# Kernel optimization log

Hardware: AMD Instinct MI355X
Metric: run time of the kernel (lower is better)

Reference implementation:

```python
import jax, jax.numpy as jnp
import numpy as np

HID = 2048          # hidden_size
INTER = 4096        # expand * hidden_size
NH = 64             # num_heads
HD = 64             # head_dim (NH*HD == INTER)
N = 128             # ssm state_size
G = 1               # n_groups
K = 4               # conv_kernel
EPS = 1e-5
CONV_DIM = INTER + 2 * G * N            # 4352
PROJ = INTER + CONV_DIM + NH            # 8512 (d_mlp == 0)


def setup_inputs() -> dict:
    key = jax.random.key(0)
    ks = jax.random.split(key, 6)
    B, S = 2, 2048
    return {
        "hidden_states": jax.random.normal(ks[0], (B, S, HID), jnp.float32),
        "in_proj_w": jax.random.normal(ks[1], (PROJ, HID), jnp.float32) * 0.02,
        "conv_w": jax.random.normal(ks[2], (CONV_DIM, 1, K), jnp.float32) * 0.1,
        "conv_b": jax.random.normal(ks[3], (CONV_DIM,), jnp.float32) * 0.02,
        "dt_bias": jnp.ones((NH,), jnp.float32),
        "A_log": jnp.log(jnp.arange(1, NH + 1, dtype=jnp.float32)),
        "D": jnp.ones((NH,), jnp.float32),
        "norm_weight": jnp.ones((INTER,), jnp.float32),
        "out_proj_w": jax.random.normal(ks[4], (HID, INTER), jnp.float32) * 0.02,
    }


def _mamba2_forward(hidden_states, in_proj_w, conv_w, conv_b, dt_bias,
                    A_log, D, norm_weight, out_proj_w):
    b, sq, _ = hidden_states.shape
    # in_proj (d_mlp == 0, so split is gate | hidden_B_C | dt)
    proj = hidden_states @ in_proj_w.T                       # [b, s, PROJ]
    gate, hbc, dt = jnp.split(proj, [INTER, INTER + CONV_DIM], axis=-1)

    # causal depthwise conv1d over time + SiLU
    xc = jnp.transpose(hbc, (0, 2, 1))                       # [b, conv_dim, s]
    xc = jax.lax.conv_general_dilated(xc, conv_w, (1,), [(K - 1, 0)],
                                      feature_group_count=CONV_DIM)
    xc = xc + conv_b[None, :, None]
    hbc = jax.nn.silu(jnp.transpose(xc, (0, 2, 1)))          # [b, s, conv_dim]

    hs, Bm, Cm = jnp.split(hbc, [INTER, INTER + G * N], axis=-1)
    hs = hs.reshape(b, sq, NH, HD)
    Bm = jnp.repeat(Bm.reshape(b, sq, G, N), NH // G, axis=2)   # [b, s, nh, n]
    Cm = jnp.repeat(Cm.reshape(b, sq, G, N), NH // G, axis=2)

    A = -jnp.exp(A_log)                                      # [nh]
    dt = jax.nn.softplus(dt + dt_bias)                       # [b, s, nh]

    # selective SSM scan: state_t = exp(dt*A)*state_{t-1} + dt*B_t x_t^T
    def step(state, inp):
        xt, Bt, Ct, dtt = inp                                # [b,nh,hd],[b,nh,n],[b,nh,n],[b,nh]
        dA = jnp.exp(dtt * A)                                # [b, nh]
        state = state * dA[..., None, None] \
            + (dtt[..., None] * xt)[..., None] * Bt[:, :, None, :]
        y = jnp.einsum('bhdn,bhn->bhd', state, Ct)
        return state, y

    init = jnp.zeros((b, NH, HD, N), jnp.float32)
    xs = (jnp.moveaxis(hs, 1, 0), jnp.moveaxis(Bm, 1, 0),
          jnp.moveaxis(Cm, 1, 0), jnp.moveaxis(dt, 1, 0))
    _, ys = jax.lax.scan(step, init, xs)                     # [s, b, nh, hd]
    y = jnp.moveaxis(ys, 0, 1) + D[None, None, :, None] * hs
    y = y.reshape(b, sq, INTER)

    # gated RMSNorm (norm_before_gate=False): gate first, then normalize
    y = y * jax.nn.silu(gate)
    var = jnp.mean(y * y, axis=-1, keepdims=True)
    y = y * jax.lax.rsqrt(var + EPS) * norm_weight
    return y @ out_proj_w.T                                  # [b, s, HID]


def reference(hidden_states, in_proj_w, conv_w, conv_b, dt_bias, A_log, D,
              norm_weight, out_proj_w):
    return _mamba2_forward(hidden_states, in_proj_w, conv_w, conv_b, dt_bias,
                           A_log, D, norm_weight, out_proj_w)
```

## Files before the change

kernel.cpp:

```cpp
#include <hip/hip_runtime.h>
#include <hip/hip_bf16.h>
#include <cstddef>
#include <cstdint>

#define HID   2048
#define INTER 4096
#define NH    64
#define HD    64
#define NST   128
#define CONV_DIM 4352
#define PROJ  8512
#define PROJ_PAD 8704
#define SS    2048
#define BB    2
#define BS    (BB*SS)
#define EPS   1e-5f

#define COL_HS 4096
#define COL_B  8192
#define COL_C  8320
#define COL_DT 8448

#define NCHC  64
#define CHUNKC 32
#define CV8   (CONV_DIM / 8)

#define CL    128
#define NCHK  16

typedef short s16x8 __attribute__((ext_vector_type(8)));
typedef float f32x4 __attribute__((ext_vector_type(4)));

__device__ inline ushort f2b(float x) {
  __hip_bfloat16 h = __float2bfloat16(x);
  return *(ushort*)&h;
}
__device__ inline float b2f(ushort u) {
  unsigned int v = ((unsigned int)u) << 16;
  return __uint_as_float(v);
}
__device__ inline int swz(int row, int e) { return row * 128 + (e ^ ((row & 7) << 3)); }

__device__ inline void gload16(const void* g, void* l) {
  __builtin_amdgcn_global_load_lds((const __attribute__((address_space(1))) void*)g,
                                   (__attribute__((address_space(3))) void*)l, 16, 0, 0);
}

#define N4A  ((long)BS * HID / 4)
#define N4W1 ((long)PROJ_PAD * HID / 4)
#define N4W2 ((long)HID * INTER / 4)

__global__ __launch_bounds__(256) void convert_all(
    const float* __restrict__ hs, const float* __restrict__ w1,
    const float* __restrict__ w2, ushort* __restrict__ hs16,
    ushort* __restrict__ w1p, ushort* __restrict__ w216) {
  long i = (long)blockIdx.x * 256 + threadIdx.x;
  const float* src;
  ushort* dst;
  long e0;
  if (i < N4A) {
    src = hs; dst = hs16; e0 = i * 4;
  } else if (i < N4A + N4W1) {
    long k = i - N4A;
    e0 = k * 4;
    long row = e0 >> 11;
    if (row >= PROJ) {
      ushort4 z = {0, 0, 0, 0};
      *(ushort4*)(w1p + e0) = z;
      return;
    }
    src = w1; dst = w1p;
  } else if (i < N4A + N4W1 + N4W2) {
    long k = i - N4A - N4W1;
    src = w2; dst = w216; e0 = k * 4;
  } else {
    return;
  }
  float4 v = *(const float4*)(src + e0);
  ushort4 o;
  o.x = f2b(v.x); o.y = f2b(v.y); o.z = f2b(v.z); o.w = f2b(v.w);
  *(ushort4*)(dst + e0) = o;
}

__global__ __launch_bounds__(512, 2) void gemm1_256x128(
    const ushort* __restrict__ A, const ushort* __restrict__ Bw,
    ushort* __restrict__ C, float* __restrict__ dtbuf) {
  __shared__ ushort smem[49152];
  const int tid = threadIdx.x;
  const int lane = tid & 63;
  const int wid = tid >> 6;
  const int wm = wid >> 1;
  const int wn = wid & 1;
  const int r = lane & 15;
  const int kx = lane >> 4;

  const int fid = blockIdx.x;
  const int rg = fid / 272;
  const int ix = fid % 272;
  const int brow = rg * 4 + (ix & 3);
  const int bcol = ix >> 2;

  const ushort* Ag = A + (size_t)(brow * 256) * HID;
  const ushort* Bg = Bw + (size_t)(bcol * 128) * HID;

  const int srow = tid >> 3;
  const int scole = (((tid & 7) * 16) ^ ((srow & 7) << 4)) >> 1;

  auto stageA1 = [&](int buf, int kt) {
#pragma unroll
    for (int i = 0; i < 4; i++) {
      gload16(Ag + (size_t)(i * 64 + srow) * HID + kt * 64 + scole,
              smem + buf * 16384 + i * 4096 + tid * 8);
    }
  };
  auto stageB1 = [&](int buf, int kt) {
#pragma unroll
    for (int i = 0; i < 2; i++) {
      gload16(Bg + (size_t)(i * 64 + srow) * HID + kt * 64 + scole,
              smem + 32768 + buf * 8192 + i * 4096 + tid * 8);
    }
  };
  auto ldA1 = [&](int buf, int mf, int ks) -> s16x8 {
    int row = wm * 64 + mf * 16 + r;
    int cb = (ks * 64 + kx * 16) ^ ((row & 7) << 4);
    return *(const s16x8*)(smem + buf * 16384 + row * 64 + (cb >> 1));
  };
  auto ldB1 = [&](int buf, int nf, int ks) -> s16x8 {
    int row = wn * 64 + nf * 16 + r;
    int cb = (ks * 64 + kx * 16) ^ ((row & 7) << 4);
    return *(const s16x8*)(smem + 32768 + buf * 8192 + row * 64 + (cb >> 1));
  };

  f32x4 acc[4][4];
#pragma unroll
  for (int i = 0; i < 4; i++)
#pragma unroll
    for (int j = 0; j < 4; j++) acc[i][j] = (f32x4)0.f;

  constexpr int NT = HID / 64;

  stageA1(0, 0); stageB1(0, 0);
  stageA1(1, 1); stageB1(1, 1);
  asm volatile("s_waitcnt vmcnt(6)" ::: "memory");
  __builtin_amdgcn_s_barrier();

  int cur = 0;
  for (int t = 0; t < NT; t++) {
    s16x8 a[4][2], b[4][2];
#pragma unroll
    for (int mf = 0; mf < 4; mf++)
#pragma unroll
      for (int ks = 0; ks < 2; ks++) a[mf][ks] = ldA1(cur, mf, ks);
#pragma unroll
    for (int nf = 0; nf < 4; nf++)
#pragma unroll
      for (int ks = 0; ks < 2; ks++) b[nf][ks] = ldB1(cur, nf, ks);
    __builtin_amdgcn_s_barrier();
    asm volatile("s_waitcnt lgkmcnt(0)" ::: "memory");
    __builtin_amdgcn_sched_barrier(0);
    __builtin_amdgcn_s_setprio(1);
#pragma unroll
    for (int mf = 0; mf < 4; mf++)
#pragma unroll
      for (int nf = 0; nf < 2; nf++)
#pragma unroll
        for (int ks = 0; ks < 2; ks++)
          acc[mf][nf] = __builtin_amdgcn_mfma_f32_16x16x32_bf16(a[mf][ks], b[nf][ks], acc[mf][nf], 0, 0, 0);
    __builtin_amdgcn_s_setprio(0);
    __builtin_amdgcn_s_barrier();
    if (t + 2 < NT) { stageA1(cur, t + 2); stageB1(cur, t + 2); }
    __builtin_amdgcn_s_setprio(1);
#pragma unroll
    for (int mf = 0; mf < 4; mf++)
#pragma unroll
      for (int nf = 2; nf < 4; nf++)
#pragma unroll
        for (int ks = 0; ks < 2; ks++)
          acc[mf][nf] = __builtin_amdgcn_mfma_f32_16x16x32_bf16(a[mf][ks], b[nf][ks], acc[mf][nf], 0, 0, 0);
    __builtin_amdgcn_s_setprio(0);
    if (t + 2 < NT) {
      asm volatile("s_waitcnt vmcnt(6)" ::: "memory");
    } else {
      asm volatile("s_waitcnt vmcnt(0)" ::: "memory");
    }
    __builtin_amdgcn_s_barrier();
    cur ^= 1;
  }

  const int m0 = brow * 256 + wm * 64 + (lane >> 4) * 4;
  const int n0 = bcol * 128 + wn * 64 + r;
#pragma unroll
  for (int mf = 0; mf < 4; mf++) {
#pragma unroll
    for (int nf = 0; nf < 4; nf++) {
      int n = n0 + nf * 16;
      if (n >= PROJ) continue;
#pragma unroll
      for (int q = 0; q < 4; q++) {
        float v = acc[mf][nf][q];
        int m = m0 + mf * 16 + q;
        C[(size_t)m * PROJ + n] = f2b(v);
        if (n >= COL_DT) dtbuf[(size_t)m * 64 + (n - COL_DT)] = v;
      }
    }
  }
}

__global__ __launch_bounds__(512, 2) void gemm2_256x128(
    const ushort* __restrict__ A, const ushort* __restrict__ Bw,
    float* __restrict__ C) {
  __shared__ ushort smem[49152];
  const int tid = threadIdx.x;
  const int lane = tid & 63;
  const int wid = tid >> 6;
  const int wm = wid >> 1;
  const int wn = wid & 1;
  const int r = lane & 15;
  const int kx = lane >> 4;

  const int fid = blockIdx.x;
  const int bcol = fid >> 4;
  const int brow = fid & 15;

  const ushort* Ag = A + (size_t)(brow * 256) * PROJ;
  const ushort* Bg = Bw + (size_t)(bcol * 128) * INTER;

  const int srow = tid >> 3;
  const int scole = (((tid & 7) * 16) ^ ((srow & 7) << 4)) >> 1;

  auto stageA2 = [&](int buf, int kt) {
#pragma unroll
    for (int i = 0; i < 4; i++) {
      gload16(Ag + (size_t)(i * 64 + srow) * PROJ + kt * 64 + scole,
              smem + buf * 16384 + i * 4096 + tid * 8);
    }
  };
  auto stageB2 = [&](int buf, int kt) {
#pragma unroll
    for (int i = 0; i < 2; i++) {
      gload16(Bg + (size_t)(i * 64 + srow) * INTER + kt * 64 + scole,
              smem + 32768 + buf * 8192 + i * 4096 + tid * 8);
    }
  };
  auto ldA2 = [&](int buf, int mf, int ks) -> s16x8 {
    int row = wm * 64 + mf * 16 + r;
    int cb = (ks * 64 + kx * 16) ^ ((row & 7) << 4);
    return *(const s16x8*)(smem + buf * 16384 + row * 64 + (cb >> 1));
  };
  auto ldB2 = [&](int buf, int nf, int ks) -> s16x8 {
    int row = wn * 64 + nf * 16 + r;
    int cb = (ks * 64 + kx * 16) ^ ((row & 7) << 4);
    return *(const s16x8*)(smem + 32768 + buf * 8192 + row * 64 + (cb >> 1));
  };

  f32x4 acc[4][4];
#pragma unroll
  for (int i = 0; i < 4; i++)
#pragma unroll
    for (int j = 0; j < 4; j++) acc[i][j] = (f32x4)0.f;

  constexpr int NT = INTER / 64;

  stageA2(0, 0); stageB2(0, 0);
  stageA2(1, 1); stageB2(1, 1);
  asm volatile("s_waitcnt vmcnt(6)" ::: "memory");
  __builtin_amdgcn_s_barrier();

  int cur = 0;
  for (int t = 0; t < NT; t++) {
    s16x8 a[4][2], b[4][2];
#pragma unroll
    for (int mf = 0; mf < 4; mf++)
#pragma unroll
      for (int ks = 0; ks < 2; ks++) a[mf][ks] = ldA2(cur, mf, ks);
#pragma unroll
    for (int nf = 0; nf < 4; nf++)
#pragma unroll
      for (int ks = 0; ks < 2; ks++) b[nf][ks] = ldB2(cur, nf, ks);
    __builtin_amdgcn_s_barrier();
    asm volatile("s_waitcnt lgkmcnt(0)" ::: "memory");
    __builtin_amdgcn_sched_barrier(0);
    __builtin_amdgcn_s_setprio(1);
#pragma unroll
    for (int mf = 0; mf < 4; mf++)
#pragma unroll
      for (int nf = 0; nf < 2; nf++)
#pragma unroll
        for (int ks = 0; ks < 2; ks++)
          acc[mf][nf] = __builtin_amdgcn_mfma_f32_16x16x32_bf16(a[mf][ks], b[nf][ks], acc[mf][nf], 0, 0, 0);
    __builtin_amdgcn_s_setprio(0);
    __builtin_amdgcn_s_barrier();
    if (t + 2 < NT) { stageA2(cur, t + 2); stageB2(cur, t + 2); }
    __builtin_amdgcn_s_setprio(1);
#pragma unroll
    for (int mf = 0; mf < 4; mf++)
#pragma unroll
      for (int nf = 2; nf < 4; nf++)
#pragma unroll
        for (int ks = 0; ks < 2; ks++)
          acc[mf][nf] = __builtin_amdgcn_mfma_f32_16x16x32_bf16(a[mf][ks], b[nf][ks], acc[mf][nf], 0, 0, 0);
    __builtin_amdgcn_s_setprio(0);
    if (t + 2 < NT) {
      asm volatile("s_waitcnt vmcnt(6)" ::: "memory");
    } else {
      asm volatile("s_waitcnt vmcnt(0)" ::: "memory");
    }
    __builtin_amdgcn_s_barrier();
    cur ^= 1;
  }

  const int m0 = brow * 256 + wm * 64 + (lane >> 4) * 4;
  const int n0 = bcol * 128 + wn * 64 + r;
#pragma unroll
  for (int mf = 0; mf < 4; mf++) {
#pragma unroll
    for (int nf = 0; nf < 4; nf++) {
      int n = n0 + nf * 16;
#pragma unroll
      for (int q = 0; q < 4; q++)
        C[(size_t)(m0 + mf * 16 + q) * HID + n] = acc[mf][nf][q];
    }
  }
}

__global__ __launch_bounds__(256) void conv_capture(
    const ushort* __restrict__ proj, ushort* __restrict__ side) {
  int idx = blockIdx.x * 256 + threadIdx.x;
  const int total = BB * NCHC * 3 * CV8;
  if (idx >= total) return;
  int c8 = idx % CV8;
  int t = idx / CV8;
  int j = t % 3; t /= 3;
  int chunk = t % NCHC;
  int b = t / NCHC;
  int s = chunk * CHUNKC - 1 - j;
  s16x8 v = {0, 0, 0, 0, 0, 0, 0, 0};
  if (s >= 0) v = *(const s16x8*)(proj + ((size_t)b * SS + s) * PROJ + COL_HS + c8 * 8);
  *(s16x8*)(side + ((size_t)(b * NCHC + chunk) * 3 + j) * CONV_DIM + c8 * 8) = v;
}

__global__ __launch_bounds__(256) void conv_silu(
    ushort* __restrict__ proj, const ushort* __restrict__ side,
    const float* __restrict__ cw, const float* __restrict__ cb) {
  int idx = blockIdx.x * 256 + threadIdx.x;
  const int total = BB * NCHC * CV8;
  if (idx >= total) return;
  int c8 = idx % CV8;
  int t = idx / CV8;
  int chunk = t % NCHC;
  int b = t / NCHC;
  const int c0 = c8 * 8;
  float w0[8], w1[8], w2[8], w3[8], bias[8], h1[8], h2[8], h3[8];
#pragma unroll
  for (int e = 0; e < 8; e++) {
    float4 wv = *(const float4*)(cw + (c0 + e) * 4);
    w0[e] = wv.x; w1[e] = wv.y; w2[e] = wv.z; w3[e] = wv.w;
    bias[e] = cb[c0 + e];
  }
  const ushort* sd = side + (size_t)(b * NCHC + chunk) * 3 * CONV_DIM;
  {
    s16x8 v1 = *(const s16x8*)(sd + c0);
    s16x8 v2 = *(const s16x8*)(sd + CONV_DIM + c0);
    s16x8 v3 = *(const s16x8*)(sd + 2 * CONV_DIM + c0);
#pragma unroll
    for (int e = 0; e < 8; e++) {
      h1[e] = b2f((ushort)v1[e]);
      h2[e] = b2f((ushort)v2[e]);
      h3[e] = b2f((ushort)v3[e]);
    }
  }
  size_t p = ((size_t)b * SS + (size_t)chunk * CHUNKC) * PROJ + COL_HS + c0;
  for (int s = 0; s < CHUNKC; s++) {
    s16x8 xv = *(const s16x8*)(proj + p);
    s16x8 ov;
#pragma unroll
    for (int e = 0; e < 8; e++) {
      float x = b2f((ushort)xv[e]);
      float o = w3[e] * x + w2[e] * h1[e] + w1[e] * h2[e] + w0[e] * h3[e] + bias[e];
      o = o / (1.f + __expf(-o));
      ov[e] = (short)f2b(o);
      h3[e] = h2[e]; h2[e] = h1[e]; h1[e] = x;
    }
    *(s16x8*)(proj + p) = ov;
    p += PROJ;
  }
}

__global__ __launch_bounds__(256) void ssd_chunk_state(
    const ushort* __restrict__ proj, const float* __restrict__ dtf,
    const float* __restrict__ dt_bias, const float* __restrict__ A_log,
    ushort* __restrict__ states, float* __restrict__ cumbuf,
    float* __restrict__ dtvbuf) {
  const int bid = blockIdx.x;
  const int c = bid & 15;
  const int h = (bid >> 4) & 63;
  const int b = bid >> 10;
  const int tid = threadIdx.x;
  const int lane = tid & 63;
  const int wv = tid >> 6;
  __shared__ float sdtv[CL], scum[CL], sw[CL];
  __shared__ ushort sBt[128 * 128];
  __shared__ ushort sXw[64 * 128];
  const size_t row0 = (size_t)b * SS + (size_t)c * CL;
  const size_t bh = (size_t)(b * NH + h);

  const float Ah = -__expf(A_log[h]);
  if (tid < CL) {
    float z = dtf[(row0 + tid) * 64 + h] + dt_bias[h];
    float dtv = (z > 20.f) ? z : log1pf(__expf(z));
    sdtv[tid] = dtv;
    sw[tid] = dtv * Ah;
  }
  __syncthreads();
  for (int off = 1; off < CL; off <<= 1) {
    float v = 0.f;
    if (tid < CL) { v = sw[tid]; if (tid >= off) v += sw[tid - off]; }
    __syncthreads();
    if (tid < CL) sw[tid] = v;
    __syncthreads();
  }
  if (tid < CL) {
    scum[tid] = sw[tid];
    cumbuf[bh * SS + c * CL + tid] = sw[tid];
    dtvbuf[bh * SS + c * CL + tid] = sdtv[tid];
  }
  __syncthreads();
  const float cumL = scum[CL - 1];
  if (tid < CL) sw[tid] = __expf(cumL - scum[tid]) * sdtv[tid];
  __syncthreads();

  {
    const int t = tid >> 1, n0 = (tid & 1) * 64;
    const ushort* src = proj + (row0 + t) * PROJ + COL_B + n0;
#pragma unroll
    for (int j = 0; j < 64; j += 8) {
      s16x8 v = *(const s16x8*)(src + j);
#pragma unroll
      for (int e = 0; e < 8; e++) sBt[swz(n0 + j + e, t)] = (ushort)v[e];
    }
  }
  {
    const int d = tid & 63;
    const int t0 = (tid >> 6) * 32;
    for (int t = t0; t < t0 + 32; t++) {
      float x = b2f(proj[(row0 + t) * PROJ + COL_HS + h * 64 + d]);
      sXw[swz(d, t)] = f2b(x * sw[t]);
    }
  }
  __syncthreads();

  const int r = lane & 15, kx = lane >> 4;
  f32x4 acc[2][4];
#pragma unroll
  for (int i = 0; i < 2; i++)
#pragma unroll
    for (int j = 0; j < 4; j++) acc[i][j] = (f32x4)0.f;
#pragma unroll
  for (int kk = 0; kk < 4; kk++) {
    s16x8 a[2], bo[4];
#pragma unroll
    for (int i = 0; i < 2; i++)
      a[i] = *(const s16x8*)&sBt[swz(wv * 32 + i * 16 + r, kk * 32 + kx * 8)];
#pragma unroll
    for (int j = 0; j < 4; j++)
      bo[j] = *(const s16x8*)&sXw[swz(j * 16 + r, kk * 32 + kx * 8)];
#pragma unroll
    for (int i = 0; i < 2; i++)
#pragma unroll
      for (int j = 0; j < 4; j++)
        acc[i][j] = __builtin_amdgcn_mfma_f32_16x16x32_bf16(a[i], bo[j], acc[i][j], 0, 0, 0);
  }
  ushort* dst = states + (size_t)bid * (128 * 64);
#pragma unroll
  for (int i = 0; i < 2; i++) {
#pragma unroll
    for (int j = 0; j < 4; j++) {
      int n = wv * 32 + i * 16 + (lane >> 4) * 4;
      int d = (lane & 15) + j * 16;
      ushort4 o;
      o.x = f2b(acc[i][j][0]);
      o.y = f2b(acc[i][j][1]);
      o.z = f2b(acc[i][j][2]);
      o.w = f2b(acc[i][j][3]);
      *(ushort4*)(dst + (size_t)d * 128 + n) = o;
    }
  }
}

__global__ __launch_bounds__(256) void ssd_state_scan(
    ushort* __restrict__ states, const float* __restrict__ cumbuf) {
  const int bh = blockIdx.x;
  const int tid = threadIdx.x;
  float run[32];
#pragma unroll
  for (int i = 0; i < 32; i++) run[i] = 0.f;
  for (int c = 0; c < NCHK; c++) {
    float dec = __expf(cumbuf[(size_t)bh * SS + c * CL + (CL - 1)]);
    ushort* p = states + ((size_t)bh * NCHK + c) * 8192 + tid * 32;
    s16x8 in[4];
#pragma unroll
    for (int v = 0; v < 4; v++) in[v] = *(const s16x8*)(p + v * 8);
    s16x8 out[4];
#pragma unroll
    for (int v = 0; v < 4; v++) {
#pragma unroll
      for (int e = 0; e < 8; e++) {
        int i = v * 8 + e;
        out[v][e] = (short)f2b(run[i]);
        run[i] = dec * run[i] + b2f((ushort)in[v][e]);
      }
    }
#pragma unroll
    for (int v = 0; v < 4; v++) *(s16x8*)(p + v * 8) = out[v];
  }
}

__global__ __launch_bounds__(256, 2) void ssd_chunk_out(
    ushort* __restrict__ proj, const ushort* __restrict__ states,
    const float* __restrict__ cumbuf, const float* __restrict__ dtvbuf,
    const float* __restrict__ Dp) {
  const int bid = blockIdx.x;
  const int c = bid & 15;
  const int h = (bid >> 4) & 63;
  const int b = bid >> 10;
  const int tid = threadIdx.x;
  const int lane = tid & 63;
  const int wv = tid >> 6;
  __shared__ ushort sC[128 * 128];
  __shared__ ushort sB[128 * 128];
  __shared__ ushort sX[64 * 128];
  const size_t row0 = (size_t)b * SS + (size_t)c * CL;
  const size_t bh = (size_t)(b * NH + h);
  const float* cumb = cumbuf + bh * SS + c * CL;
  const float* dtvb = dtvbuf + bh * SS + c * CL;
  const int r = lane & 15, kx = lane >> 4;

  float ct[2][4];
#pragma unroll
  for (int i = 0; i < 2; i++)
#pragma unroll
    for (int q = 0; q < 4; q++)
      ct[i][q] = cumb[wv * 32 + i * 16 + ((lane >> 4) << 2) + q];
  float cumt[8], dvt[8];
#pragma unroll
  for (int j = 0; j < 8; j++) {
    int tau = j * 16 + (lane & 15);
    cumt[j] = cumb[tau];
    dvt[j] = dtvb[tau];
  }
  const float eC = __expf(cumb[wv * 32 + (lane >> 1)]);

  {
    const int t = tid >> 1, n0 = (tid & 1) * 64;
    const ushort* srcC = proj + (row0 + t) * PROJ + COL_C + n0;
    const ushort* srcB = proj + (row0 + t) * PROJ + COL_B + n0;
#pragma unroll
    for (int j = 0; j < 64; j += 8) {
      *(s16x8*)&sC[swz(t, n0 + j)] = *(const s16x8*)(srcC + j);
      *(s16x8*)&sB[swz(t, n0 + j)] = *(const s16x8*)(srcB + j);
    }
  }
  {
    const int d = tid & 63;
    const int t0 = (tid >> 6) * 32;
    for (int t = t0; t < t0 + 32; t++)
      sX[swz(d, t)] = proj[(row0 + t) * PROJ + COL_HS + h * 64 + d];
  }
  __syncthreads();

  f32x4 g[2][8];
#pragma unroll
  for (int i = 0; i < 2; i++)
#pragma unroll
    for (int j = 0; j < 8; j++) g[i][j] = (f32x4)0.f;
#pragma unroll
  for (int kk = 0; kk < 4; kk++) {
    s16x8 a[2], bo[8];
#pragma unroll
    for (int i = 0; i < 2; i++)
      a[i] = *(const s16x8*)&sC[swz(wv * 32 + i * 16 + r, kk * 32 + kx * 8)];
#pragma unroll
    for (int j = 0; j < 8; j++)
      bo[j] = *(const s16x8*)&sB[swz(j * 16 + r, kk * 32 + kx * 8)];
#pragma unroll
    for (int i = 0; i < 2; i++)
#pragma unroll
      for (int j = 0; j < 8; j++)
        g[i][j] = __builtin_amdgcn_mfma_f32_16x16x32_bf16(a[i], bo[j], g[i][j], 0, 0, 0);
  }

  s16x8 spf[4][4];
  {
    const ushort* sp = states + (size_t)bid * 8192;
#pragma unroll
    for (int kk = 0; kk < 4; kk++)
#pragma unroll
      for (int j = 0; j < 4; j++)
        spf[kk][j] = *(const s16x8*)(sp + (size_t)(j * 16 + r) * 128 + kk * 32 + kx * 8);
  }
  __syncthreads();

#pragma unroll
  for (int j = 0; j < 8; j++) {
    float cu = cumt[j], dv = dvt[j];
    int tau = j * 16 + (lane & 15);
#pragma unroll
    for (int i = 0; i < 2; i++) {
#pragma unroll
      for (int q = 0; q < 4; q++) {
        int t = wv * 32 + i * 16 + ((lane >> 4) << 2) + q;
        float val = (tau <= t) ? g[i][j][q] * __expf(ct[i][q] - cu) * dv : 0.f;
        sB[swz(t, tau)] = f2b(val);
      }
    }
  }
  {
    int t = wv * 32 + (lane >> 1);
    int n0 = (lane & 1) * 64;
#pragma unroll
    for (int j = 0; j < 64; j += 8) {
      s16x8 u = *(const s16x8*)&sC[swz(t, n0 + j)];
#pragma unroll
      for (int k = 0; k < 8; k++) u[k] = (short)f2b(b2f((ushort)u[k]) * eC);
      *(s16x8*)&sC[swz(t, n0 + j)] = u;
    }
  }
  __syncthreads();

  f32x4 y[2][4];
#pragma unroll
  for (int i = 0; i < 2; i++)
#pragma unroll
    for (int j = 0; j < 4; j++) y[i][j] = (f32x4)0.f;
#pragma unroll
  for (int kk = 0; kk < 4; kk++) {
    s16x8 a[2], bo[4];
#pragma unroll
    for (int i = 0; i < 2; i++)
      a[i] = *(const s16x8*)&sB[swz(wv * 32 + i * 16 + r, kk * 32 + kx * 8)];
#pragma unroll
    for (int j = 0; j < 4; j++)
      bo[j] = *(const s16x8*)&sX[swz(j * 16 + r, kk * 32 + kx * 8)];
#pragma unroll
    for (int i = 0; i < 2; i++)
#pragma unroll
      for (int j = 0; j < 4; j++)
        y[i][j] = __builtin_amdgcn_mfma_f32_16x16x32_bf16(a[i], bo[j], y[i][j], 0, 0, 0);
  }
#pragma unroll
  for (int kk = 0; kk < 4; kk++) {
    s16x8 a[2];
#pragma unroll
    for (int i = 0; i < 2; i++)
      a[i] = *(const s16x8*)&sC[swz(wv * 32 + i * 16 + r, kk * 32 + kx * 8)];
#pragma unroll
    for (int i = 0; i < 2; i++)
#pragma unroll
      for (int j = 0; j < 4; j++)
        y[i][j] = __builtin_amdgcn_mfma_f32_16x16x32_bf16(a[i], spf[kk][j], y[i][j], 0, 0, 0);
  }

  const float Dh = Dp[h];
#pragma unroll
  for (int i = 0; i < 2; i++) {
#pragma unroll
    for (int j = 0; j < 4; j++) {
      int t0 = wv * 32 + i * 16 + (lane >> 4) * 4;
      int d = (lane & 15) + j * 16;
#pragma unroll
      for (int q = 0; q < 4; q++) {
        float x = b2f(sX[swz(d, t0 + q)]);
        proj[(row0 + t0 + q) * PROJ + COL_HS + h * 64 + d] = f2b(y[i][j][q] + Dh * x);
      }
    }
  }
}

__global__ __launch_bounds__(256) void rmsnorm_kernel(
    ushort* __restrict__ proj, const float* __restrict__ nw) {
  const int row = blockIdx.x;
  const int tid = threadIdx.x;
  ushort* yp = proj + (size_t)row * PROJ + COL_HS;
  const ushort* gp = proj + (size_t)row * PROJ;
  float v[16];
  float ss = 0.f;
#pragma unroll
  for (int q = 0; q < 4; q++) {
    int col = q * 1024 + tid * 4;
    ushort4 yv = *(const ushort4*)(yp + col);
    ushort4 gv = *(const ushort4*)(gp + col);
    float vy[4] = {b2f(yv.x), b2f(yv.y), b2f(yv.z), b2f(yv.w)};
    float vg[4] = {b2f(gv.x), b2f(gv.y), b2f(gv.z), b2f(gv.w)};
#pragma unroll
    for (int j = 0; j < 4; j++) {
      float sg = vg[j] / (1.f + __expf(-vg[j]));
      float vv = vy[j] * sg;
      v[q * 4 + j] = vv;
      ss += vv * vv;
    }
  }
#pragma unroll
  for (int o = 1; o < 64; o <<= 1) ss += __shfl_xor(ss, o);
  __shared__ float red[4];
  if ((tid & 63) == 0) red[tid >> 6] = ss;
  __syncthreads();
  float tot = red[0] + red[1] + red[2] + red[3];
  float scale = rsqrtf(tot * (1.f / INTER) + EPS);
#pragma unroll
  for (int q = 0; q < 4; q++) {
    int col = q * 1024 + tid * 4;
    float4 w = *(const float4*)(nw + col);
    ushort4 o;
    o.x = f2b(v[q * 4 + 0] * scale * w.x);
    o.y = f2b(v[q * 4 + 1] * scale * w.y);
    o.z = f2b(v[q * 4 + 2] * scale * w.z);
    o.w = f2b(v[q * 4 + 3] * scale * w.w);
    *(ushort4*)(yp + col) = o;
  }
}

extern "C" void kernel_launch(void* const* d_in, const int* in_sizes, int n_in,
                              void* d_out, int out_size, void* d_ws, size_t ws_size,
                              hipStream_t stream) {
  const float* hs   = (const float*)d_in[0];
  const float* w1   = (const float*)d_in[1];
  const float* cw   = (const float*)d_in[2];
  const float* cb   = (const float*)d_in[3];
  const float* dtb  = (const float*)d_in[4];
  const float* alog = (const float*)d_in[5];
  const float* Dp   = (const float*)d_in[6];
  const float* nw   = (const float*)d_in[7];
  const float* w2   = (const float*)d_in[8];
  float* out = (float*)d_out;

  char* base = (char*)d_ws;
  size_t off = 0;
  ushort* proj = (ushort*)(base + off); off += (size_t)BS * PROJ * 2;
  ushort* side = (ushort*)(base + off); off += (size_t)BB * NCHC * 3 * CONV_DIM * 2;
  off = (off + 255) & ~(size_t)255;
  float* dtbuf = (float*)(base + off); off += (size_t)BS * 64 * 4;
  off = (off + 255) & ~(size_t)255;
  ushort* w216 = (ushort*)(base + off); off += (size_t)HID * INTER * 2;
  off = (off + 255) & ~(size_t)255;
  char* rC = base + off;
  ushort* hs16 = (ushort*)rC;
  ushort* w1p  = (ushort*)(rC + 16777216);
  ushort* states = (ushort*)rC;
  float*  cumbuf = (float*)(rC + 33554432);
  float*  dtvbuf = (float*)(rC + 33554432 + 1048576);

  {
    long n4 = N4A + N4W1 + N4W2;
    convert_all<<<(int)((n4 + 255) / 256), 256, 0, stream>>>(hs, w1, w2, hs16, w1p, w216);
  }

  gemm1_256x128<<<1088, 512, 0, stream>>>(hs16, w1p, proj, dtbuf);

  conv_capture<<<(BB * NCHC * 3 * CV8 + 255) / 256, 256, 0, stream>>>(proj, side);
  conv_silu<<<(BB * NCHC * CV8 + 255) / 256, 256, 0, stream>>>(proj, side, cw, cb);

  ssd_chunk_state<<<BB * NH * NCHK, 256, 0, stream>>>(proj, dtbuf, dtb, alog, states, cumbuf, dtvbuf);
  ssd_state_scan<<<BB * NH, 256, 0, stream>>>(states, cumbuf);
  ssd_chunk_out<<<BB * NH * NCHK, 256, 0, stream>>>(proj, states, cumbuf, dtvbuf, Dp);

  rmsnorm_kernel<<<BS, 256, 0, stream>>>(proj, nw);

  gemm2_256x128<<<256, 512, 0, stream>>>(
      (const ushort*)(proj + COL_HS), w216, out);
}
```

Measured before the change: 440.1 us.

## Enlarge in_proj GEMM tile to 256x256, wave-shuffle dt scan, register C in chunk_out

The in_proj GEMM moves from 256x128 to 256x256 tiles with 8 waves in a 2x4 layout and an 8-phase schedule that interleaves LDS reads, MFMA groups and staged global loads. This raises arithmetic intensity per block and halves the grid. The chunk-state kernel swaps its barrier-heavy shared-memory prefix sum for wave shuffles. The chunk-output kernel loads C fragments directly into registers, drops the sC shared buffer and the rescale pass, and applies exp(cum) to a separate inter-chunk accumulator in fp32. The larger tile uses more LDS and accumulator registers, which may reduce occupancy.

```diff
diff --git a/kernel.cpp b/kernel.cpp
--- a/kernel.cpp
+++ b/kernel.cpp
@@ -82,79 +82,77 @@
   *(ushort4*)(dst + e0) = o;
 }
 
-__global__ __launch_bounds__(512, 2) void gemm1_256x128(
+__global__ __launch_bounds__(512, 2) void gemm256_8ph(
     const ushort* __restrict__ A, const ushort* __restrict__ Bw,
     ushort* __restrict__ C, float* __restrict__ dtbuf) {
-  __shared__ ushort smem[49152];
+  __shared__ ushort smem[65536];
   const int tid = threadIdx.x;
   const int lane = tid & 63;
   const int wid = tid >> 6;
-  const int wm = wid >> 1;
-  const int wn = wid & 1;
+  const int wm = wid >> 2;
+  const int wn = wid & 3;
   const int r = lane & 15;
   const int kx = lane >> 4;
 
   const int fid = blockIdx.x;
-  const int rg = fid / 272;
-  const int ix = fid % 272;
-  const int brow = rg * 4 + (ix & 3);
-  const int bcol = ix >> 2;
+  const int bcol = ((fid >> 7) << 3) + ((fid & 127) >> 4);
+  const int brow = fid & 15;
 
   const ushort* Ag = A + (size_t)(brow * 256) * HID;
-  const ushort* Bg = Bw + (size_t)(bcol * 128) * HID;
+  const ushort* Bg = Bw + (size_t)(bcol * 256) * HID;
 
   const int srow = tid >> 3;
   const int scole = (((tid & 7) * 16) ^ ((srow & 7) << 4)) >> 1;
 
-  auto stageA1 = [&](int buf, int kt) {
-#pragma unroll
-    for (int i = 0; i < 4; i++) {
-      gload16(Ag + (size_t)(i * 64 + srow) * HID + kt * 64 + scole,
-              smem + buf * 16384 + i * 4096 + tid * 8);
-    }
+  auto stageA = [&](int buf, int kt, int half) {
+    const ushort* g = Ag + (size_t)(half * 128 + srow) * HID + kt * 64 + scole;
+    ushort* l = smem + buf * 16384 + half * 8192 + tid * 8;
+    gload16(g, l);
+    gload16(g + (size_t)64 * HID, l + 4096);
   };
-  auto stageB1 = [&](int buf, int kt) {
-#pragma unroll
-    for (int i = 0; i < 2; i++) {
-      gload16(Bg + (size_t)(i * 64 + srow) * HID + kt * 64 + scole,
-              smem + 32768 + buf * 8192 + i * 4096 + tid * 8);
-    }
+  auto stageB = [&](int buf, int kt, int half) {
+    const ushort* g = Bg + (size_t)(half * 128 + srow) * HID + kt * 64 + scole;
+    ushort* l = smem + 32768 + buf * 16384 + half * 8192 + tid * 8;
+    gload16(g, l);
+    gload16(g + (size_t)64 * HID, l + 4096);
   };
-  auto ldA1 = [&](int buf, int mf, int ks) -> s16x8 {
-    int row = wm * 64 + mf * 16 + r;
+  auto ldA = [&](int buf, int mf, int ks) -> s16x8 {
+    int row = wm * 128 + mf * 16 + r;
     int cb = (ks * 64 + kx * 16) ^ ((row & 7) << 4);
     return *(const s16x8*)(smem + buf * 16384 + row * 64 + (cb >> 1));
   };
-  auto ldB1 = [&](int buf, int nf, int ks) -> s16x8 {
+  auto ldB = [&](int buf, int nf, int ks) -> s16x8 {
     int row = wn * 64 + nf * 16 + r;
     int cb = (ks * 64 + kx * 16) ^ ((row & 7) << 4);
-    return *(const s16x8*)(smem + 32768 + buf * 8192 + row * 64 + (cb >> 1));
+    return *(const s16x8*)(smem + 32768 + buf * 16384 + row * 64 + (cb >> 1));
   };
 
-  f32x4 acc[4][4];
-#pragma unroll
-  for (int i = 0; i < 4; i++)
+  f32x4 acc[8][4];
+#pragma unroll
+  for (int i = 0; i < 8; i++)
 #pragma unroll
     for (int j = 0; j < 4; j++) acc[i][j] = (f32x4)0.f;
 
   constexpr int NT = HID / 64;
 
-  stageA1(0, 0); stageB1(0, 0);
-  stageA1(1, 1); stageB1(1, 1);
-  asm volatile("s_waitcnt vmcnt(6)" ::: "memory");
+  stageA(0, 0, 0); stageA(0, 0, 1);
+  stageB(0, 0, 0); stageB(0, 0, 1);
+  stageA(1, 1, 0); stageA(1, 1, 1);
+  asm volatile("s_waitcnt vmcnt(4)" ::: "memory");
   __builtin_amdgcn_s_barrier();
 
   int cur = 0;
   for (int t = 0; t < NT; t++) {
-    s16x8 a[4][2], b[4][2];
-#pragma unroll
-    for (int mf = 0; mf < 4; mf++)
-#pragma unroll
-      for (int ks = 0; ks < 2; ks++) a[mf][ks] = ldA1(cur, mf, ks);
-#pragma unroll
-    for (int nf = 0; nf < 4; nf++)
-#pragma unroll
-      for (int ks = 0; ks < 2; ks++) b[nf][ks] = ldB1(cur, nf, ks);
+    s16x8 a[4][2], b[2][2], b2[2][2];
+#pragma unroll
+    for (int mf = 0; mf < 4; mf++)
+#pragma unroll
+      for (int ks = 0; ks < 2; ks++) a[mf][ks] = ldA(cur, mf, ks);
+#pragma unroll
+    for (int nf = 0; nf < 2; nf++)
+#pragma unroll
+      for (int ks = 0; ks < 2; ks++) b[nf][ks] = ldB(cur, nf, ks);
+    if (t + 1 < NT) stageB(cur ^ 1, t + 1, 0);
     __builtin_amdgcn_s_barrier();
     asm volatile("s_waitcnt lgkmcnt(0)" ::: "memory");
     __builtin_amdgcn_sched_barrier(0);
@@ -168,18 +166,53 @@
           acc[mf][nf] = __builtin_amdgcn_mfma_f32_16x16x32_bf16(a[mf][ks], b[nf][ks], acc[mf][nf], 0, 0, 0);
     __builtin_amdgcn_s_setprio(0);
     __builtin_amdgcn_s_barrier();
-    if (t + 2 < NT) { stageA1(cur, t + 2); stageB1(cur, t + 2); }
+#pragma unroll
+    for (int nf = 0; nf < 2; nf++)
+#pragma unroll
+      for (int ks = 0; ks < 2; ks++) b2[nf][ks] = ldB(cur, nf + 2, ks);
+    if (t + 1 < NT) stageB(cur ^ 1, t + 1, 1);
+    __builtin_amdgcn_s_barrier();
+    asm volatile("s_waitcnt lgkmcnt(0)" ::: "memory");
+    __builtin_amdgcn_sched_barrier(0);
     __builtin_amdgcn_s_setprio(1);
 #pragma unroll
     for (int mf = 0; mf < 4; mf++)
 #pragma unroll
-      for (int nf = 2; nf < 4; nf++)
+      for (int nf = 0; nf < 2; nf++)
 #pragma unroll
         for (int ks = 0; ks < 2; ks++)
-          acc[mf][nf] = __builtin_amdgcn_mfma_f32_16x16x32_bf16(a[mf][ks], b[nf][ks], acc[mf][nf], 0, 0, 0);
+          acc[mf][nf + 2] = __builtin_amdgcn_mfma_f32_16x16x32_bf16(a[mf][ks], b2[nf][ks], acc[mf][nf + 2], 0, 0, 0);
+    __builtin_amdgcn_s_setprio(0);
+    __builtin_amdgcn_s_barrier();
+#pragma unroll
+    for (int mf = 0; mf < 4; mf++)
+#pragma unroll
+      for (int ks = 0; ks < 2; ks++) a[mf][ks] = ldA(cur, mf + 4, ks);
+    __builtin_amdgcn_s_barrier();
+    asm volatile("s_waitcnt lgkmcnt(0)" ::: "memory");
+    __builtin_amdgcn_sched_barrier(0);
+    __builtin_amdgcn_s_setprio(1);
+#pragma unroll
+    for (int mf = 0; mf < 4; mf++)
+#pragma unroll
+      for (int nf = 0; nf < 2; nf++)
+#pragma unroll
+        for (int ks = 0; ks < 2; ks++)
+          acc[mf + 4][nf] = __builtin_amdgcn_mfma_f32_16x16x32_bf16(a[mf][ks], b[nf][ks], acc[mf + 4][nf], 0, 0, 0);
+    __builtin_amdgcn_s_setprio(0);
+    __builtin_amdgcn_s_barrier();
+    if (t + 2 < NT) { stageA(cur, t + 2, 0); stageA(cur, t + 2, 1); }
+    __builtin_amdgcn_s_setprio(1);
+#pragma unroll
+    for (int mf = 0; mf < 4; mf++)
+#pragma unroll
+      for (int nf = 0; nf < 2; nf++)
+#pragma unroll
+        for (int ks = 0; ks < 2; ks++)
+          acc[mf + 4][nf + 2] = __builtin_amdgcn_mfma_f32_16x16x32_bf16(a[mf][ks], b2[nf][ks], acc[mf + 4][nf + 2], 0, 0, 0);
     __builtin_amdgcn_s_setprio(0);
     if (t + 2 < NT) {
-      asm volatile("s_waitcnt vmcnt(6)" ::: "memory");
+      asm volatile("s_waitcnt vmcnt(4)" ::: "memory");
     } else {
       asm volatile("s_waitcnt vmcnt(0)" ::: "memory");
     }
@@ -187,10 +220,10 @@
     cur ^= 1;
   }
 
-  const int m0 = brow * 256 + wm * 64 + (lane >> 4) * 4;
-  const int n0 = bcol * 128 + wn * 64 + r;
-#pragma unroll
-  for (int mf = 0; mf < 4; mf++) {
+  const int m0 = brow * 256 + wm * 128 + (lane >> 4) * 4;
+  const int n0 = bcol * 256 + wn * 64 + r;
+#pragma unroll
+  for (int mf = 0; mf < 8; mf++) {
 #pragma unroll
     for (int nf = 0; nf < 4; nf++) {
       int n = n0 + nf * 16;
@@ -399,34 +432,36 @@
   const int lane = tid & 63;
   const int wv = tid >> 6;
   __shared__ float sdtv[CL], scum[CL], sw[CL];
+  __shared__ float wtot[2];
   __shared__ ushort sBt[128 * 128];
   __shared__ ushort sXw[64 * 128];
   const size_t row0 = (size_t)b * SS + (size_t)c * CL;
   const size_t bh = (size_t)(b * NH + h);
 
   const float Ah = -__expf(A_log[h]);
+  float dtvv = 0.f, v = 0.f;
   if (tid < CL) {
     float z = dtf[(row0 + tid) * 64 + h] + dt_bias[h];
-    float dtv = (z > 20.f) ? z : log1pf(__expf(z));
-    sdtv[tid] = dtv;
-    sw[tid] = dtv * Ah;
-  }
+    dtvv = (z > 20.f) ? z : log1pf(__expf(z));
+    v = dtvv * Ah;
+  }
+#pragma unroll
+  for (int off = 1; off < 64; off <<= 1) {
+    float u = __shfl_up(v, off);
+    if (lane >= off) v += u;
+  }
+  if (tid < CL && lane == 63) wtot[wv] = v;
   __syncthreads();
-  for (int off = 1; off < CL; off <<= 1) {
-    float v = 0.f;
-    if (tid < CL) { v = sw[tid]; if (tid >= off) v += sw[tid - off]; }
-    __syncthreads();
-    if (tid < CL) sw[tid] = v;
-    __syncthreads();
-  }
+  if (wv == 1) v += wtot[0];
   if (tid < CL) {
-    scum[tid] = sw[tid];
-    cumbuf[bh * SS + c * CL + tid] = sw[tid];
-    dtvbuf[bh * SS + c * CL + tid] = sdtv[tid];
+    sdtv[tid] = dtvv;
+    scum[tid] = v;
+    cumbuf[bh * SS + c * CL + tid] = v;
+    dtvbuf[bh * SS + c * CL + tid] = dtvv;
   }
   __syncthreads();
   const float cumL = scum[CL - 1];
-  if (tid < CL) sw[tid] = __expf(cumL - scum[tid]) * sdtv[tid];
+  if (tid < CL) sw[tid] = __expf(cumL - v) * dtvv;
   __syncthreads();
 
   {
@@ -434,9 +469,9 @@
     const ushort* src = proj + (row0 + t) * PROJ + COL_B + n0;
 #pragma unroll
     for (int j = 0; j < 64; j += 8) {
-      s16x8 v = *(const s16x8*)(src + j);
-#pragma unroll
-      for (int e = 0; e < 8; e++) sBt[swz(n0 + j + e, t)] = (ushort)v[e];
+      s16x8 vv = *(const s16x8*)(src + j);
+#pragma unroll
+      for (int e = 0; e < 8; e++) sBt[swz(n0 + j + e, t)] = (ushort)vv[e];
     }
   }
   {
@@ -526,7 +561,6 @@
   const int tid = threadIdx.x;
   const int lane = tid & 63;
   const int wv = tid >> 6;
-  __shared__ ushort sC[128 * 128];
   __shared__ ushort sB[128 * 128];
   __shared__ ushort sX[64 * 128];
   const size_t row0 = (size_t)b * SS + (size_t)c * CL;
@@ -548,17 +582,13 @@
     cumt[j] = cumb[tau];
     dvt[j] = dtvb[tau];
   }
-  const float eC = __expf(cumb[wv * 32 + (lane >> 1)]);
 
   {
     const int t = tid >> 1, n0 = (tid & 1) * 64;
-    const ushort* srcC = proj + (row0 + t) * PROJ + COL_C + n0;
     const ushort* srcB = proj + (row0 + t) * PROJ + COL_B + n0;
 #pragma unroll
-    for (int j = 0; j < 64; j += 8) {
-      *(s16x8*)&sC[swz(t, n0 + j)] = *(const s16x8*)(srcC + j);
+    for (int j = 0; j < 64; j += 8)
       *(s16x8*)&sB[swz(t, n0 + j)] = *(const s16x8*)(srcB + j);
-    }
   }
   {
     const int d = tid & 63;
@@ -566,6 +596,13 @@
     for (int t = t0; t < t0 + 32; t++)
       sX[swz(d, t)] = proj[(row0 + t) * PROJ + COL_HS + h * 64 + d];
   }
+  s16x8 cf[4][2];
+#pragma unroll
+  for (int kk = 0; kk < 4; kk++)
+#pragma unroll
+    for (int i = 0; i < 2; i++)
+      cf[kk][i] = *(const s16x8*)(proj + (row0 + wv * 32 + i * 16 + r) * PROJ
+                                  + COL_C + kk * 32 + kx * 8);
   __syncthreads();
 
   f32x4 g[2][8];
@@ -575,10 +612,7 @@
     for (int j = 0; j < 8; j++) g[i][j] = (f32x4)0.f;
 #pragma unroll
   for (int kk = 0; kk < 4; kk++) {
-    s16x8 a[2], bo[8];
-#pragma unroll
-    for (int i = 0; i < 2; i++)
-      a[i] = *(const s16x8*)&sC[swz(wv * 32 + i * 16 + r, kk * 32 + kx * 8)];
+    s16x8 bo[8];
 #pragma unroll
     for (int j = 0; j < 8; j++)
       bo[j] = *(const s16x8*)&sB[swz(j * 16 + r, kk * 32 + kx * 8)];
@@ -586,17 +620,28 @@
     for (int i = 0; i < 2; i++)
 #pragma unroll
       for (int j = 0; j < 8; j++)
-        g[i][j] = __builtin_amdgcn_mfma_f32_16x16x32_bf16(a[i], bo[j], g[i][j], 0, 0, 0);
-  }
-
-  s16x8 spf[4][4];
+        g[i][j] = __builtin_amdgcn_mfma_f32_16x16x32_bf16(cf[kk][i], bo[j], g[i][j], 0, 0, 0);
+  }
+
+  f32x4 yi[2][4];
+#pragma unroll
+  for (int i = 0; i < 2; i++)
+#pragma unroll
+    for (int j = 0; j < 4; j++) yi[i][j] = (f32x4)0.f;
   {
     const ushort* sp = states + (size_t)bid * 8192;
 #pragma unroll
-    for (int kk = 0; kk < 4; kk++)
+    for (int kk = 0; kk < 4; kk++) {
+      s16x8 spk[4];
 #pragma unroll
       for (int j = 0; j < 4; j++)
-        spf[kk][j] = *(const s16x8*)(sp + (size_t)(j * 16 + r) * 128 + kk * 32 + kx * 8);
+        spk[j] = *(const s16x8*)(sp + (size_t)(j * 16 + r) * 128 + kk * 32 + kx * 8);
+#pragma unroll
+      for (int i = 0; i < 2; i++)
+#pragma unroll
+        for (int j = 0; j < 4; j++)
+          yi[i][j] = __builtin_amdgcn_mfma_f32_16x16x32_bf16(cf[kk][i], spk[j], yi[i][j], 0, 0, 0);
+    }
   }
   __syncthreads();
 
@@ -614,17 +659,6 @@
       }
     }
   }
-  {
-    int t = wv * 32 + (lane >> 1);
-    int n0 = (lane & 1) * 64;
-#pragma unroll
-    for (int j = 0; j < 64; j += 8) {
-      s16x8 u = *(const s16x8*)&sC[swz(t, n0 + j)];
-#pragma unroll
-      for (int k = 0; k < 8; k++) u[k] = (short)f2b(b2f((ushort)u[k]) * eC);
-      *(s16x8*)&sC[swz(t, n0 + j)] = u;
-    }
-  }
   __syncthreads();
 
   f32x4 y[2][4];
@@ -647,20 +681,13 @@
       for (int j = 0; j < 4; j++)
         y[i][j] = __builtin_amdgcn_mfma_f32_16x16x32_bf16(a[i], bo[j], y[i][j], 0, 0, 0);
   }
-#pragma unroll
-  for (int kk = 0; kk < 4; kk++) {
-    s16x8 a[2];
-#pragma unroll
-    for (int i = 0; i < 2; i++)
-      a[i] = *(const s16x8*)&sC[swz(wv * 32 + i * 16 + r, kk * 32 + kx * 8)];
-#pragma unroll
-    for (int i = 0; i < 2; i++)
-#pragma unroll
-      for (int j = 0; j < 4; j++)
-        y[i][j] = __builtin_amdgcn_mfma_f32_16x16x32_bf16(a[i], spf[kk][j], y[i][j], 0, 0, 0);
-  }
 
   const float Dh = Dp[h];
+  float eP[2][4];
+#pragma unroll
+  for (int i = 0; i < 2; i++)
+#pragma unroll
+    for (int q = 0; q < 4; q++) eP[i][q] = __expf(ct[i][q]);
 #pragma unroll
   for (int i = 0; i < 2; i++) {
 #pragma unroll
@@ -670,7 +697,8 @@
 #pragma unroll
       for (int q = 0; q < 4; q++) {
         float x = b2f(sX[swz(d, t0 + q)]);
-        proj[(row0 + t0 + q) * PROJ + COL_HS + h * 64 + d] = f2b(y[i][j][q] + Dh * x);
+        proj[(row0 + t0 + q) * PROJ + COL_HS + h * 64 + d] =
+            f2b(y[i][j][q] + eP[i][q] * yi[i][j][q] + Dh * x);
       }
     }
   }
@@ -754,7 +782,7 @@
     convert_all<<<(int)((n4 + 255) / 256), 256, 0, stream>>>(hs, w1, w2, hs16, w1p, w216);
   }
 
-  gemm1_256x128<<<1088, 512, 0, stream>>>(hs16, w1p, proj, dtbuf);
+  gemm256_8ph<<<(BS / 256) * (PROJ_PAD / 256), 512, 0, stream>>>(hs16, w1p, proj, dtbuf);
 
   conv_capture<<<(BB * NCHC * 3 * CV8 + 255) / 256, 256, 0, stream>>>(proj, side);
   conv_silu<<<(BB * NCHC * CV8 + 255) / 256, 256, 0, stream>>>(proj, side, cw, cb);
```

After: 430.7 us. 2.1% less time.
